# Performance work log

Measured on AMD Instinct MI355X. Metric: run time of the kernel, lower is better.

## Reference

```python
import jax, jax.numpy as jnp
import numpy as np

B, S, DM = 4, 2048, 1024
H, HD = 16, 64  # num_heads, head_dimension


def setup_inputs() -> dict:
    key = jax.random.key(0)
    ks = jax.random.split(key, 11)
    s = 0.02
    return {
        "queries": jax.random.normal(ks[0], (B, S, DM), dtype=jnp.float32),
        "keys": jax.random.normal(ks[1], (B, S, DM), dtype=jnp.float32),
        "values": jax.random.normal(ks[2], (B, S, DM), dtype=jnp.float32),
        # projection params, stored [in, out] (transpose of torch Linear weight)
        "Wq": jax.random.normal(ks[3], (DM, H * HD), dtype=jnp.float32) * s,
        "bq": jnp.zeros((H * HD,), dtype=jnp.float32),
        "Wk": jax.random.normal(ks[4], (DM, H * HD), dtype=jnp.float32) * s,
        "bk": jnp.zeros((H * HD,), dtype=jnp.float32),
        "Wv": jax.random.normal(ks[5], (DM, H * HD), dtype=jnp.float32) * s,
        "bv": jnp.zeros((H * HD,), dtype=jnp.float32),
        "Wo": jax.random.normal(ks[6], (H * HD, DM), dtype=jnp.float32) * s,
        "bo": jnp.zeros((DM,), dtype=jnp.float32),
    }


def reference(queries, keys, values, Wq, bq, Wk, bk, Wv, bv, Wo, bo):
    b, s, _ = queries.shape
    # project and split heads: [b, s, H*HD] -> [b, H, s, HD]
    def split(x):
        return x.reshape(b, s, H, HD).transpose(0, 2, 1, 3)
    q = split(queries @ Wq + bq)
    k = split(keys @ Wk + bk)
    v = split(values @ Wv + bv)
    # raw scores [b, H, sq, sk]
    attn = jnp.einsum("bhqd,bhkd->bhqk", q, k)
    # FAITHFUL to source: mask is a no-op (masked_fill result discarded);
    # softmax over axis=2 (the QUERY axis), then scaled by 1/sqrt(HD) after.
    attn = jax.nn.softmax(attn, axis=2) / jnp.sqrt(jnp.float32(HD))
    out = jnp.einsum("bhqk,bhkd->bhqd", attn, v)  # [b, H, s, HD]
    out = out.transpose(0, 2, 1, 3).reshape(b, s, H * HD)
    return out @ Wo + bo
```

## Files before the change

### kernel.cpp

```cpp
#include <hip/hip_runtime.h>
#include <cstddef>


typedef unsigned short u16t;
typedef __attribute__((ext_vector_type(8))) short short8;
typedef __attribute__((ext_vector_type(4))) float floatx4;
typedef __attribute__((ext_vector_type(4))) unsigned int uintx4;

#define MFMA16(a, b, c) __builtin_amdgcn_mfma_f32_16x16x32_bf16((a), (b), (c), 0, 0, 0)
#define GLDS16(g, l)                                                        \
  __builtin_amdgcn_global_load_lds(                                         \
      (const __attribute__((address_space(1))) unsigned int*)(g),           \
      (__attribute__((address_space(3))) unsigned int*)(l), 16, 0, 0)
#define GLDS4(g, l)                                                         \
  __builtin_amdgcn_global_load_lds(                                         \
      (const __attribute__((address_space(1))) unsigned int*)(g),           \
      (__attribute__((address_space(3))) unsigned int*)(l), 4, 0, 0)

#if __has_builtin(__builtin_amdgcn_exp2f)
#define EXP2(x) __builtin_amdgcn_exp2f(x)
#else
#define EXP2(x) __expf(0.69314718f * (x))
#endif

static __device__ __forceinline__ u16t f2bf(float f) {
  union { float f; unsigned u; } v; v.f = f;
  unsigned r = v.u + 0x7FFFu + ((v.u >> 16) & 1u);
  return (u16t)(r >> 16);
}
static __device__ __forceinline__ unsigned pack2(float hi, float lo) {
  union { float f; unsigned u; } a, b; a.f = hi; b.f = lo;
  return __builtin_amdgcn_perm(a.u + 0x8000u, b.u + 0x8000u, 0x07060302u);
}
static __device__ __forceinline__ unsigned cvtpk(float lo, float hi) {
  unsigned r;
  asm("v_cvt_pk_bf16_f32 %0, %1, %2" : "=v"(r) : "v"(lo), "v"(hi));
  return r;
}

static __device__ __forceinline__ int swz(int row, int col) {
  return (((col >> 3) ^ (row & 7)) << 3) | (col & 7);
}

#define SEQ    2048
#define NHEAD  16
#define HDIM   64
#define DMODEL 1024

__global__ __launch_bounds__(256)
void wt_kernel(const float* __restrict__ W0, const float* __restrict__ W1,
               const float* __restrict__ W2, const float* __restrict__ W3,
               u16t* __restrict__ T0, u16t* __restrict__ T1,
               u16t* __restrict__ T2, u16t* __restrict__ T3) {
  int id = blockIdx.x * 256 + threadIdx.x;
  int wsel = id >> 17;
  int r = id & 131071;
  int n = r & 1023;
  int k0 = (r >> 10) << 3;
  const float* W = wsel == 0 ? W0 : wsel == 1 ? W1 : wsel == 2 ? W2 : W3;
  u16t* T = wsel == 0 ? T0 : wsel == 1 ? T1 : wsel == 2 ? T2 : T3;
  const float* src = W + (size_t)k0 * 1024 + n;
  float f[8];
#pragma unroll
  for (int i = 0; i < 8; ++i) f[i] = src[(size_t)i * 1024];
  uint4 p;
  p.x = pack2(f[1], f[0]); p.y = pack2(f[3], f[2]);
  p.z = pack2(f[5], f[4]); p.w = pack2(f[7], f[6]);
  *(uint4*)&T[(size_t)n * 1024 + (k0 & ~63) + swz(n, k0 & 63)] = p;
}

__global__ __launch_bounds__(256)
void proj_kernel(const float* __restrict__ Qf, const float* __restrict__ Kf,
                 const float* __restrict__ Vf,
                 const u16t* __restrict__ WQ, const u16t* __restrict__ WK,
                 const u16t* __restrict__ WV,
                 const float* __restrict__ bq, const float* __restrict__ bk,
                 const float* __restrict__ bv,
                 u16t* __restrict__ Qb, u16t* __restrict__ Kb,
                 u16t* __restrict__ Vt) {
  constexpr int K = 1024;
  __shared__ __align__(16) u16t lA[128 * 64];
  __shared__ __align__(16) u16t lB[128 * 64];
  const int z = blockIdx.z;
  const float* Ag = z == 0 ? Qf : z == 1 ? Kf : Vf;
  const u16t* BT = z == 0 ? WQ : z == 1 ? WK : WV;
  const float* bias = z == 0 ? bq : z == 1 ? bk : bv;
  const float qsc = z == 0 ? 1.44269504f : 1.0f;
  const int tid = threadIdx.x;
  const int lane = tid & 63, w = tid >> 6;
  const int wm = w >> 1, wn = w & 1;
  const int lrow = lane & 15, lq = lane >> 4;
  const int raw = blockIdx.y * 8 + blockIdx.x;
  const int xcd = raw & 7, slot = raw >> 3;
  const int m0 = (xcd * 8 + (slot >> 3)) * 128;
  const int n0 = (slot & 7) * 128;

  floatx4 acc[4][4];
#pragma unroll
  for (int i = 0; i < 4; ++i)
#pragma unroll
    for (int j = 0; j < 4; ++j) acc[i][j] = {0.f, 0.f, 0.f, 0.f};

  for (int kb = 0; kb < K; kb += 64) {
#pragma unroll
    for (int i = 0; i < 8; ++i) {
      int e = (i * 256 + tid) * 4;
      int r = e >> 6, c = e & 63;
      const float* src = Ag + (size_t)(m0 + r) * K + kb + c;
      uint2 p;
      p.x = pack2(src[1], src[0]);
      p.y = pack2(src[3], src[2]);
      *(uint2*)&lA[r * 64 + swz(r, c)] = p;
    }
#pragma unroll
    for (int i = 0; i < 4; ++i) {
      int chunk = w * 4 + i;
      int off = chunk * 1024 + lane * 16;
      int r = off >> 7, ib = off & 127;
      GLDS16(BT + (size_t)(n0 + r) * K + kb + (ib >> 1), &lB[chunk * 512]);
    }
    __syncthreads();
#pragma unroll
    for (int kk = 0; kk < 2; ++kk) {
      short8 af[4], bfr[4];
#pragma unroll
      for (int t = 0; t < 4; ++t) {
        int ar = wm * 64 + t * 16 + lrow;
        af[t] = *(const short8*)&lA[ar * 64 + swz(ar, kk * 32 + lq * 8)];
      }
#pragma unroll
      for (int t = 0; t < 4; ++t) {
        int br = wn * 64 + t * 16 + lrow;
        bfr[t] = *(const short8*)&lB[br * 64 + swz(br, kk * 32 + lq * 8)];
      }
#pragma unroll
      for (int i = 0; i < 4; ++i)
#pragma unroll
        for (int j = 0; j < 4; ++j)
          acc[i][j] = MFMA16(af[i], bfr[j], acc[i][j]);
    }
    __syncthreads();
  }

  float bvv[4];
#pragma unroll
  for (int j = 0; j < 4; ++j) bvv[j] = bias[n0 + wn * 64 + j * 16 + lrow];
  const int h = (n0 + wn * 64) >> 6;
  u16t* Out = z == 0 ? Qb : Kb;
#pragma unroll
  for (int i = 0; i < 4; ++i) {
#pragma unroll
    for (int r = 0; r < 4; ++r) {
      int rg = m0 + wm * 64 + i * 16 + lq * 4 + r;
      int b = rg >> 11, s = rg & 2047;
      size_t bh = (size_t)(b * NHEAD + h);
#pragma unroll
      for (int j = 0; j < 4; ++j) {
        int cg = n0 + wn * 64 + j * 16 + lrow;
        int d = cg & 63;
        float v = acc[i][j][r] + bvv[j];
        if (z < 2) {
          Out[(bh * SEQ + s) * HDIM + swz(s, d)] = f2bf(v * qsc);
        } else {
          int sp = (s & ~31) | (((s >> 2) & 3) << 3) | (s & 3) |
                   (((s >> 4) & 1) << 2);
          Vt[(bh * HDIM + d) * SEQ + (s & ~127) + swz(d, sp & 127)] = f2bf(v);
        }
      }
    }
  }
}

__global__ __launch_bounds__(256)
void stats_kernel(const u16t* __restrict__ Qb, const u16t* __restrict__ Kb,
                  float* __restrict__ lss) {
  __shared__ __align__(16) u16t lK[128 * 64];
  __shared__ __align__(16) u16t lQ[128 * 64];
  const int tid = threadIdx.x, lane = tid & 63, w = tid >> 6;
  const int lrow = lane & 15, lq = lane >> 4;
  const int bh = blockIdx.x;
  const int c0 = blockIdx.y * 128;
  const u16t* Kbase = Kb + (size_t)bh * (SEQ * HDIM);
  const u16t* Qbase = Qb + (size_t)bh * (SEQ * HDIM);

#pragma unroll
  for (int i = 0; i < 4; ++i) {
    int chunk = w * 4 + i;
    GLDS16(Kbase + (size_t)c0 * HDIM + chunk * 512 + lane * 8, &lK[chunk * 512]);
  }

  short8 bfK[4];
  float lcur[2] = {0.f, 0.f};

  for (int q0 = 0; q0 < SEQ; q0 += 128) {
#pragma unroll
    for (int i = 0; i < 4; ++i) {
      int chunk = w * 4 + i;
      GLDS16(Qbase + (size_t)q0 * HDIM + chunk * 512 + lane * 8, &lQ[chunk * 512]);
    }
    __syncthreads();
    if (q0 == 0) {
#pragma unroll
      for (int nt = 0; nt < 2; ++nt) {
        int kr = w * 32 + nt * 16 + lrow;
        bfK[nt * 2]     = *(const short8*)&lK[kr * 64 + swz(kr, lq * 8)];
        bfK[nt * 2 + 1] = *(const short8*)&lK[kr * 64 + swz(kr, lq * 8 + 32)];
      }
    }
#pragma unroll
    for (int mt = 0; mt < 8; ++mt) {
      int qr = mt * 16 + lrow;
      short8 af0 = *(const short8*)&lQ[qr * 64 + swz(qr, lq * 8)];
      short8 af1 = *(const short8*)&lQ[qr * 64 + swz(qr, lq * 8 + 32)];
#pragma unroll
      for (int nt = 0; nt < 2; ++nt) {
        floatx4 a = {0.f, 0.f, 0.f, 0.f};
        a = MFMA16(af0, bfK[nt * 2], a);
        a = MFMA16(af1, bfK[nt * 2 + 1], a);
        lcur[nt] += EXP2(a[0]) + EXP2(a[1]) + EXP2(a[2]) + EXP2(a[3]);
      }
    }
    __syncthreads();
  }
#pragma unroll
  for (int t = 0; t < 2; ++t) {
    float ll = lcur[t];
    ll += __shfl_xor(ll, 16);
    ll += __shfl_xor(ll, 32);
    lcur[t] = ll;
  }
  if (lane < 16) {
#pragma unroll
    for (int t = 0; t < 2; ++t) {
      int col = c0 + w * 32 + t * 16 + lane;
      lss[(size_t)bh * SEQ + col] = -3.0f - __log2f(lcur[t]);
    }
  }
}

__global__ __launch_bounds__(256, 2)
void attn_kernel(const u16t* __restrict__ Qb, const u16t* __restrict__ Kb,
                 const u16t* __restrict__ Vt, const float* __restrict__ Lb,
                 u16t* __restrict__ Hout) {
  __shared__ __align__(16) u16t sK[2][8192];
  __shared__ __align__(16) u16t sV[2][8192];
  __shared__ __align__(16) float sL[2][128];
  const int tid = threadIdx.x, lane = tid & 63, w = tid >> 6;
  const int lrow = lane & 15, lq = lane >> 4;
  const int bh = blockIdx.x, q0 = blockIdx.y * 256;
  const size_t hb = (size_t)bh * (SEQ * HDIM);
  const float* Lg = Lb + (size_t)bh * SEQ;

  auto stage = [&](int t) {
    u16t* dK = sK[t & 1];
    u16t* dV = sV[t & 1];
    float* dL = sL[t & 1];
    const int k0 = t << 7;
#pragma unroll
    for (int i = 0; i < 4; ++i) {
      int chunk = w * 4 + i;
      GLDS16(Kb + hb + (size_t)k0 * HDIM + chunk * 512 + lane * 8, &dK[chunk * 512]);
    }
#pragma unroll
    for (int i = 0; i < 4; ++i) {
      int chunk = w * 4 + i;
      int off = chunk * 1024 + lane * 16;
      int d = off >> 8, ib = off & 255;
      GLDS16(Vt + hb + ((size_t)d << 11) + k0 + (ib >> 1), &dV[chunk * 512]);
    }
    GLDS4(Lg + k0 + lane, &dL[0]);
    GLDS4(Lg + k0 + 64 + lane, &dL[64]);
  };
  auto loadK = [&](short8 dst[2][2], const u16t* K_, int kw) {
#pragma unroll
    for (int t = 0; t < 2; ++t) {
      int kr = (kw * 2 + t) * 16 + lrow;
      dst[t][0] = *(const short8*)&K_[kr * 64 + swz(kr, lq * 8)];
      dst[t][1] = *(const short8*)&K_[kr * 64 + swz(kr, lq * 8 + 32)];
    }
  };
  auto loadV = [&](short8 dst[4], const u16t* V_, int kw) {
#pragma unroll
    for (int dt = 0; dt < 4; ++dt) {
      int vr = dt * 16 + lrow;
      dst[dt] = *(const short8*)&V_[vr * 128 + swz(vr, kw * 32 + lq * 8)];
    }
  };

  u16t* qs = (u16t*)sK;
#pragma unroll
  for (int i = 0; i < 8; ++i) {
    int chunk = w * 8 + i;
    GLDS16(Qb + hb + (size_t)q0 * HDIM + chunk * 512 + lane * 8, &qs[chunk * 512]);
  }
  __syncthreads();
  short8 bq[4][2];
#pragma unroll
  for (int j = 0; j < 4; ++j) {
    int qr = w * 64 + j * 16 + lrow;
    bq[j][0] = *(const short8*)&qs[qr * 64 + swz(qr, lq * 8)];
    bq[j][1] = *(const short8*)&qs[qr * 64 + swz(qr, lq * 8 + 32)];
  }
  __syncthreads();

  auto qk = [&](const short8 ak[2][2], floatx4 s[4][2], floatx4 cA, floatx4 cB) {
    __builtin_amdgcn_s_setprio(1);
#pragma unroll
    for (int j = 0; j < 4; ++j) {
      floatx4 a = cA, b = cB;
      a = MFMA16(ak[0][0], bq[j][0], a);
      a = MFMA16(ak[0][1], bq[j][1], a);
      b = MFMA16(ak[1][0], bq[j][0], b);
      b = MFMA16(ak[1][1], bq[j][1], b);
      s[j][0] = a; s[j][1] = b;
    }
    __builtin_amdgcn_s_setprio(0);
  };
  auto ep = [&](const floatx4 s[4][2], short8 pa[4]) {
#pragma unroll
    for (int j = 0; j < 4; ++j) {
      uintx4 pw;
      pw[0] = cvtpk(EXP2(s[j][0][0]), EXP2(s[j][0][1]));
      pw[1] = cvtpk(EXP2(s[j][0][2]), EXP2(s[j][0][3]));
      pw[2] = cvtpk(EXP2(s[j][1][0]), EXP2(s[j][1][1]));
      pw[3] = cvtpk(EXP2(s[j][1][2]), EXP2(s[j][1][3]));
      pa[j] = __builtin_bit_cast(short8, pw);
    }
  };

  floatx4 ao[4][4];
#pragma unroll
  for (int j = 0; j < 4; ++j)
#pragma unroll
    for (int t = 0; t < 4; ++t) ao[j][t] = {0.f, 0.f, 0.f, 0.f};

  stage(0);
  stage(1);

#pragma unroll 2
  for (int kt = 0; kt < 16; ++kt) {
    if (kt < 15) asm volatile("s_waitcnt vmcnt(10)" ::: "memory");
    else         asm volatile("s_waitcnt vmcnt(0)" ::: "memory");
    __builtin_amdgcn_s_barrier();
    const u16t* K_ = sK[kt & 1];
    const u16t* V_ = sV[kt & 1];
    const float* L_ = sL[kt & 1];

    short8 ak0[2][2];
    loadK(ak0, K_, 0);
    floatx4 cA = *(const floatx4*)&L_[lq * 4];
    floatx4 cB = *(const floatx4*)&L_[16 + lq * 4];
    floatx4 s0[4][2];
    qk(ak0, s0, cA, cB);
    short8 pa[4];
    ep(s0, pa);

#pragma unroll
    for (int kw = 0; kw < 4; ++kw) {
      short8 bv[4];
      loadV(bv, V_, kw);
      short8 akN[2][2];
      floatx4 sN[4][2];
      if (kw < 3) {
        loadK(akN, K_, kw + 1);
        floatx4 cAn = *(const floatx4*)&L_[(kw + 1) * 32 + lq * 4];
        floatx4 cBn = *(const floatx4*)&L_[(kw + 1) * 32 + 16 + lq * 4];
        qk(akN, sN, cAn, cBn);
      }
      __builtin_amdgcn_s_setprio(1);
#pragma unroll
      for (int dt = 0; dt < 4; ++dt)
#pragma unroll
        for (int j = 0; j < 4; ++j)
          ao[j][dt] = MFMA16(pa[j], bv[dt], ao[j][dt]);
      __builtin_amdgcn_s_setprio(0);
      if (kw < 3) {
        short8 paN[4];
        ep(sN, paN);
#pragma unroll
        for (int j = 0; j < 4; ++j) pa[j] = paN[j];
      }
    }

    asm volatile("s_waitcnt lgkmcnt(0)" ::: "memory");
    __builtin_amdgcn_s_barrier();
    if (kt < 14) stage(kt + 2);
  }

  const int b = bh >> 4, h = bh & 15;
#pragma unroll
  for (int j = 0; j < 4; ++j)
#pragma unroll
    for (int dt = 0; dt < 4; ++dt) {
      int d = dt * 16 + lrow;
#pragma unroll
      for (int r = 0; r < 4; ++r) {
        int q = q0 + w * 64 + j * 16 + lq * 4 + r;
        Hout[((size_t)b * SEQ + q) * DMODEL + h * HDIM + swz(q, d)] = f2bf(ao[j][dt][r]);
      }
    }
}

__global__ __launch_bounds__(256)
void outproj_kernel(const u16t* __restrict__ Ag, const u16t* __restrict__ BT,
                    const float* __restrict__ bias, float* __restrict__ Cp) {
  constexpr int K = 1024;
  __shared__ __align__(16) u16t lA[128 * 64];
  __shared__ __align__(16) u16t lB[128 * 64];
  const int tid = threadIdx.x;
  const int lane = tid & 63, w = tid >> 6;
  const int wm = w >> 1, wn = w & 1;
  const int lrow = lane & 15, lq = lane >> 4;
  const int raw = blockIdx.y * 8 + blockIdx.x;
  const int xcd = raw & 7, slot = raw >> 3;
  const int m0 = (xcd * 8 + (slot >> 3)) * 128;
  const int n0 = (slot & 7) * 128;

  floatx4 acc[4][4];
#pragma unroll
  for (int i = 0; i < 4; ++i)
#pragma unroll
    for (int j = 0; j < 4; ++j) acc[i][j] = {0.f, 0.f, 0.f, 0.f};

  for (int kb = 0; kb < K; kb += 64) {
#pragma unroll
    for (int i = 0; i < 4; ++i) {
      int chunk = w * 4 + i;
      int off = chunk * 1024 + lane * 16;
      int r = off >> 7, ib = off & 127;
      GLDS16(Ag + (size_t)(m0 + r) * K + kb + (ib >> 1), &lA[chunk * 512]);
      GLDS16(BT + (size_t)(n0 + r) * K + kb + (ib >> 1), &lB[chunk * 512]);
    }
    __syncthreads();
#pragma unroll
    for (int kk = 0; kk < 2; ++kk) {
      short8 af[4], bfr[4];
#pragma unroll
      for (int t = 0; t < 4; ++t) {
        int ar = wm * 64 + t * 16 + lrow;
        af[t] = *(const short8*)&lA[ar * 64 + swz(ar, kk * 32 + lq * 8)];
      }
#pragma unroll
      for (int t = 0; t < 4; ++t) {
        int br = wn * 64 + t * 16 + lrow;
        bfr[t] = *(const short8*)&lB[br * 64 + swz(br, kk * 32 + lq * 8)];
      }
#pragma unroll
      for (int i = 0; i < 4; ++i)
#pragma unroll
        for (int j = 0; j < 4; ++j)
          acc[i][j] = MFMA16(af[i], bfr[j], acc[i][j]);
    }
    __syncthreads();
  }

  float bvv[4];
#pragma unroll
  for (int j = 0; j < 4; ++j) bvv[j] = bias[n0 + wn * 64 + j * 16 + lrow];
#pragma unroll
  for (int i = 0; i < 4; ++i) {
#pragma unroll
    for (int r = 0; r < 4; ++r) {
      int rg = m0 + wm * 64 + i * 16 + lq * 4 + r;
#pragma unroll
      for (int j = 0; j < 4; ++j) {
        int cg = n0 + wn * 64 + j * 16 + lrow;
        Cp[(size_t)rg * 1024 + cg] = acc[i][j][r] + bvv[j];
      }
    }
  }
}

extern "C" void kernel_launch(void* const* d_in, const int* in_sizes, int n_in,
                              void* d_out, int out_size, void* d_ws, size_t ws_size,
                              hipStream_t stream) {
  (void)in_sizes; (void)n_in; (void)out_size; (void)ws_size;
  const float* queries = (const float*)d_in[0];
  const float* keys    = (const float*)d_in[1];
  const float* values  = (const float*)d_in[2];
  const float* Wq = (const float*)d_in[3];
  const float* bq = (const float*)d_in[4];
  const float* Wk = (const float*)d_in[5];
  const float* bk = (const float*)d_in[6];
  const float* Wv = (const float*)d_in[7];
  const float* bv = (const float*)d_in[8];
  const float* Wo = (const float*)d_in[9];
  const float* bo = (const float*)d_in[10];

  char* ws = (char*)d_ws;
  const size_t MB = 1024 * 1024;
  u16t* Qb   = (u16t*)(ws + 0 * MB);
  u16t* Kb   = (u16t*)(ws + 16 * MB);
  u16t* Hout = (u16t*)(ws + 32 * MB);
  u16t* Vt   = (u16t*)(ws + 48 * MB);
  u16t* wqt  = (u16t*)(ws + 64 * MB);
  u16t* wkt  = (u16t*)(ws + 66 * MB);
  u16t* wvt  = (u16t*)(ws + 68 * MB);
  u16t* wot  = (u16t*)(ws + 70 * MB);
  float* lss = (float*)(ws + 72 * MB);

  wt_kernel<<<2048, 256, 0, stream>>>(Wq, Wk, Wv, Wo, wqt, wkt, wvt, wot);

  proj_kernel<<<dim3(8, 64, 3), 256, 0, stream>>>(
      queries, keys, values, wqt, wkt, wvt, bq, bk, bv, Qb, Kb, Vt);

  stats_kernel<<<dim3(64, 16), 256, 0, stream>>>(Qb, Kb, lss);

  attn_kernel<<<dim3(64, 8), 256, 0, stream>>>(Qb, Kb, Vt, lss, Hout);

  outproj_kernel<<<dim3(8, 64), 256, 0, stream>>>(Hout, wot, bo, (float*)d_out);
}
```

Baseline: 378.6 us.

## Double-buffer projection GEMM with register-staged A prefetch and manual waitcnts

Restructures the projection kernel's K loop into a two-stage software pipeline. LDS buffers for A and B are doubled, fp32 A tiles are prefetched into registers two steps ahead with float4 loads, and B tiles are issued via global_load_lds into the alternate buffer. Explicit vmcnt/lgkmcnt waits and barriers replace __syncthreads, s_setprio raises priority around the MFMA block, and launch bounds request 2 blocks per CU. This aims to hide global load latency behind MFMA work, at the cost of more registers and LDS and fragile hand-counted wait values.

```diff
diff --git a/kernel.cpp b/kernel.cpp
--- a/kernel.cpp
+++ b/kernel.cpp
@@ -69,7 +69,7 @@
   *(uint4*)&T[(size_t)n * 1024 + (k0 & ~63) + swz(n, k0 & 63)] = p;
 }
 
-__global__ __launch_bounds__(256)
+__global__ __launch_bounds__(256, 2)
 void proj_kernel(const float* __restrict__ Qf, const float* __restrict__ Kf,
                  const float* __restrict__ Vf,
                  const u16t* __restrict__ WQ, const u16t* __restrict__ WK,
@@ -79,8 +79,8 @@
                  u16t* __restrict__ Qb, u16t* __restrict__ Kb,
                  u16t* __restrict__ Vt) {
   constexpr int K = 1024;
-  __shared__ __align__(16) u16t lA[128 * 64];
-  __shared__ __align__(16) u16t lB[128 * 64];
+  __shared__ __align__(16) u16t lA[2][128 * 64];
+  __shared__ __align__(16) u16t lB[2][128 * 64];
   const int z = blockIdx.z;
   const float* Ag = z == 0 ? Qf : z == 1 ? Kf : Vf;
   const u16t* BT = z == 0 ? WQ : z == 1 ? WK : WV;
@@ -95,52 +95,102 @@
   const int m0 = (xcd * 8 + (slot >> 3)) * 128;
   const int n0 = (slot & 7) * 128;
 
-  floatx4 acc[4][4];
-#pragma unroll
-  for (int i = 0; i < 4; ++i)
-#pragma unroll
-    for (int j = 0; j < 4; ++j) acc[i][j] = {0.f, 0.f, 0.f, 0.f};
-
-  for (int kb = 0; kb < K; kb += 64) {
+  auto stageA = [&](int t, float4 rA[8]) {
+    const int kb = t << 6;
 #pragma unroll
     for (int i = 0; i < 8; ++i) {
       int e = (i * 256 + tid) * 4;
       int r = e >> 6, c = e & 63;
-      const float* src = Ag + (size_t)(m0 + r) * K + kb + c;
-      uint2 p;
-      p.x = pack2(src[1], src[0]);
-      p.y = pack2(src[3], src[2]);
-      *(uint2*)&lA[r * 64 + swz(r, c)] = p;
-    }
+      rA[i] = *(const float4*)(Ag + (size_t)(m0 + r) * K + kb + c);
+    }
+  };
+  auto stageB = [&](int t) {
+    const int kb = t << 6;
+    u16t* dB = lB[t & 1];
 #pragma unroll
     for (int i = 0; i < 4; ++i) {
       int chunk = w * 4 + i;
       int off = chunk * 1024 + lane * 16;
       int r = off >> 7, ib = off & 127;
-      GLDS16(BT + (size_t)(n0 + r) * K + kb + (ib >> 1), &lB[chunk * 512]);
-    }
-    __syncthreads();
+      GLDS16(BT + (size_t)(n0 + r) * K + kb + (ib >> 1), &dB[chunk * 512]);
+    }
+  };
+  auto writeA = [&](const float4 rA[8], u16t* dA) {
+#pragma unroll
+    for (int i = 0; i < 8; ++i) {
+      int e = (i * 256 + tid) * 4;
+      int r = e >> 6, c = e & 63;
+      uint2 p;
+      p.x = pack2(rA[i].y, rA[i].x);
+      p.y = pack2(rA[i].w, rA[i].z);
+      *(uint2*)&dA[r * 64 + swz(r, c)] = p;
+    }
+  };
+
+  floatx4 acc[4][4];
+#pragma unroll
+  for (int i = 0; i < 4; ++i)
+#pragma unroll
+    for (int j = 0; j < 4; ++j) acc[i][j] = {0.f, 0.f, 0.f, 0.f};
+
+  auto compute = [&](const u16t* A_, const u16t* B_) {
 #pragma unroll
     for (int kk = 0; kk < 2; ++kk) {
       short8 af[4], bfr[4];
 #pragma unroll
       for (int t = 0; t < 4; ++t) {
         int ar = wm * 64 + t * 16 + lrow;
-        af[t] = *(const short8*)&lA[ar * 64 + swz(ar, kk * 32 + lq * 8)];
+        af[t] = *(const short8*)&A_[ar * 64 + swz(ar, kk * 32 + lq * 8)];
       }
 #pragma unroll
       for (int t = 0; t < 4; ++t) {
         int br = wn * 64 + t * 16 + lrow;
-        bfr[t] = *(const short8*)&lB[br * 64 + swz(br, kk * 32 + lq * 8)];
-      }
+        bfr[t] = *(const short8*)&B_[br * 64 + swz(br, kk * 32 + lq * 8)];
+      }
+      __builtin_amdgcn_s_setprio(1);
 #pragma unroll
       for (int i = 0; i < 4; ++i)
 #pragma unroll
         for (int j = 0; j < 4; ++j)
           acc[i][j] = MFMA16(af[i], bfr[j], acc[i][j]);
-    }
-    __syncthreads();
-  }
+      __builtin_amdgcn_s_setprio(0);
+    }
+  };
+
+  float4 rEven[8], rOdd[8];
+  stageA(0, rEven); stageB(0);
+  stageA(1, rOdd);  stageB(1);
+  asm volatile("s_waitcnt vmcnt(16)" ::: "memory");
+  writeA(rEven, lA[0]);
+
+  for (int t = 0; t < 14; t += 2) {
+    asm volatile("s_waitcnt vmcnt(12) lgkmcnt(0)" ::: "memory");
+    __builtin_amdgcn_s_barrier();
+    compute(lA[0], lB[0]);
+    asm volatile("s_waitcnt lgkmcnt(0)" ::: "memory");
+    __builtin_amdgcn_s_barrier();
+    stageA(t + 2, rEven); stageB(t + 2);
+    asm volatile("s_waitcnt vmcnt(16)" ::: "memory");
+    writeA(rOdd, lA[1]);
+    asm volatile("s_waitcnt vmcnt(12) lgkmcnt(0)" ::: "memory");
+    __builtin_amdgcn_s_barrier();
+    compute(lA[1], lB[1]);
+    asm volatile("s_waitcnt lgkmcnt(0)" ::: "memory");
+    __builtin_amdgcn_s_barrier();
+    stageA(t + 3, rOdd); stageB(t + 3);
+    asm volatile("s_waitcnt vmcnt(16)" ::: "memory");
+    writeA(rEven, lA[0]);
+  }
+  asm volatile("s_waitcnt vmcnt(12) lgkmcnt(0)" ::: "memory");
+  __builtin_amdgcn_s_barrier();
+  compute(lA[0], lB[0]);
+  asm volatile("s_waitcnt lgkmcnt(0)" ::: "memory");
+  __builtin_amdgcn_s_barrier();
+  asm volatile("s_waitcnt vmcnt(4)" ::: "memory");
+  writeA(rOdd, lA[1]);
+  asm volatile("s_waitcnt vmcnt(0) lgkmcnt(0)" ::: "memory");
+  __builtin_amdgcn_s_barrier();
+  compute(lA[1], lB[1]);
 
   float bvv[4];
 #pragma unroll
```

Result: no change. 377.3 us (-0.3%).
